# Kernel optimization log

Hardware: AMD Instinct MI355X
Metric: run time of the kernel (lower is better)

## Reference

```python
import jax, jax.numpy as jnp
import numpy as np

B, T, L, D = 4, 8, 512, 512
H, KD, VD = 8, 64, 64


def setup_inputs() -> dict:
    key = jax.random.key(0)
    ks = jax.random.split(key, 8)
    s = 0.05
    return {
        "queries": jax.random.normal(ks[0], (B, T, L, D), jnp.float32),
        "keys": jax.random.normal(ks[1], (B, T, L, D), jnp.float32),
        "values": jax.random.normal(ks[2], (B, T, L, D), jnp.float32),
        "attn_mask": jnp.ones((1, 1, 1, L, L), jnp.float32),
        "Wq": jax.random.normal(ks[3], (D, H, KD), jnp.float32) * s,
        "Wk": jax.random.normal(ks[4], (D, H, KD), jnp.float32) * s,
        "Wv": jax.random.normal(ks[5], (D, H, VD), jnp.float32) * s,
        "w_head": jax.random.normal(ks[6], (H,), jnp.float32),
        "tau": jnp.ones((1,), jnp.float32),
        "delta": jnp.zeros((1,), jnp.float32),
    }


def reference(queries, keys, values, attn_mask, Wq, Wk, Wv, w_head, tau, delta):
    # Projections: (b,t,l,d) x (d,h,e) -> (b,t,l,h,e)
    Q = jnp.einsum('btld,dhe->btlhe', queries, Wq)
    K = jnp.einsum('btld,dhe->btlhe', keys, Wk)
    V = jnp.einsum('btld,dhe->btlhe', values, Wv)
    scale = 1.0 / jnp.sqrt(jnp.asarray(KD, jnp.float32))
    # Full score tensor (b,t,h,l,s)
    scores = jnp.einsum('btlhe,btshe->bthls', Q, K)
    # de-stationary rescaling, then scale, then multiplicative mask
    scores = (scores * tau[0] + delta[0]) * scale
    scores = scores * attn_mask
    # Dropout(attn_dropout) before softmax is identity at inference
    p = jax.nn.softmax(scores, axis=-1)
    attn = jnp.einsum('bthls,btshe->bthle', p, V)
    # Per-head scalar weighted sum over heads: (b,t,h,l,e),(h)->(b,t,l,e)
    return jnp.einsum('bthle,h->btle', attn, w_head)
```

## Files before the change

kernel.cpp:

```cpp
#include <hip/hip_runtime.h>
#include <hip/hip_bf16.h>

typedef __bf16 bf16;
typedef __bf16 bf16x4 __attribute__((ext_vector_type(4)));
typedef __bf16 bf16x8 __attribute__((ext_vector_type(8)));
typedef float f32x4 __attribute__((ext_vector_type(4)));
typedef _Float16 half4 __attribute__((ext_vector_type(4)));


#if __has_builtin(__builtin_amdgcn_exp2f)
#define EXP2(x) __builtin_amdgcn_exp2f(x)
#else
#define EXP2(x) exp2f(x)
#endif

static __device__ __forceinline__ f32x4 mfma16(bf16x4 a, bf16x4 b, f32x4 c) {
#if __has_builtin(__builtin_amdgcn_mfma_f32_16x16x16bf16_1k)
    return __builtin_amdgcn_mfma_f32_16x16x16bf16_1k(a, b, c, 0, 0, 0);
#else
    asm("v_mfma_f32_16x16x16_bf16 %0, %1, %2, %0" : "+v"(c) : "v"(a), "v"(b));
    return c;
#endif
}

#if __has_builtin(__builtin_amdgcn_global_load_lds)
#define HAVE_GLL 1
#else
#define HAVE_GLL 0
#endif

static __device__ __forceinline__ void gll16(const void* gp, void* lbase, int lane) {
#if HAVE_GLL
    __builtin_amdgcn_global_load_lds(
        (const __attribute__((address_space(1))) void*)gp,
        (__attribute__((address_space(3))) void*)lbase, 16, 0, 0);
#else
    *(uint4*)((char*)lbase + lane * 16) = *(const uint4*)gp;
#endif
}

static __device__ __forceinline__ void prep_w_job(int job, const float* W0,
                                                  const float* W1, const float* W2,
                                                  bf16* Wt, char* sraw) {
    float(*t)[65] = (float(*)[65])sraw;
    const int z = job >> 6, sub = job & 63;
    const float* W = (z == 0) ? W0 : (z == 1) ? W1 : W2;
    bf16* O = Wt + (size_t)z * 512 * 512;
    const int d0 = (sub & 7) * 64, n0 = (sub >> 3) * 64;
    {
        int nl = threadIdx.x & 63, dg = threadIdx.x >> 6;
#pragma unroll
        for (int j = 0; j < 16; ++j) {
            int dl = dg + j * 4;
            t[nl][dl] = W[(size_t)(d0 + dl) * 512 + n0 + nl];
        }
    }
    __syncthreads();
    {
        int dl = threadIdx.x & 63, ng = threadIdx.x >> 6;
#pragma unroll
        for (int j = 0; j < 16; ++j) {
            int nl = ng + j * 4;
            O[(size_t)(n0 + nl) * 512 + d0 + dl] = (bf16)t[nl][dl];
        }
    }
}

static __device__ __forceinline__ void prep_mask_job(int bid, const float* maskf,
                                                     bf16* Mp) {
    const int t0 = bid * 256 + threadIdx.x;
    const float4* m4 = (const float4*)maskf;
#pragma unroll
    for (int j = 0; j < 4; ++j) {
        int idx = t0 + j * 16384;
        int q = idx >> 7;
        int sc = idx & 127;
        int cc = sc >> 4;
        int ns = (sc >> 2) & 3;
        int qd = sc & 3;
        float4 v = m4[idx];
        bf16x4 o;
        o[0] = (bf16)v.x; o[1] = (bf16)v.y; o[2] = (bf16)v.z; o[3] = (bf16)v.w;
        size_t off = ((((size_t)(q >> 4) * 8 + cc) * 4 + ns) * 4 + qd) * 64 +
                     (q & 15) * 4;
        *(bf16x4*)&Mp[off] = o;
    }
}

__global__ __launch_bounds__(256) void prep_kernel(const float* W0, const float* W1,
                                                   const float* W2, const float* maskf,
                                                   bf16* Wt, bf16* Mp) {
    __shared__ __align__(16) char sraw[16640];
    if (blockIdx.z == 3) {
        prep_mask_job(blockIdx.y * 8 + blockIdx.x, maskf, Mp);
        return;
    }
    prep_w_job(blockIdx.z * 64 + blockIdx.y * 8 + blockIdx.x, W0, W1, W2, Wt, sraw);
}

static __device__ __forceinline__ void proj_job(int j, const float* __restrict__ Xq,
                                                const float* __restrict__ Xk,
                                                const float* __restrict__ Xv,
                                                const bf16* __restrict__ Wt,
                                                bf16* __restrict__ Qw,
                                                bf16* __restrict__ Kw,
                                                bf16* __restrict__ Vt, char* sraw) {
    bf16* la = (bf16*)sraw;
    bf16* lb = (bf16*)sraw + 9216;

    const int z = j >> 9, bid = j & 511;
    const float* X = (z == 0) ? Xq : (z == 1) ? Xk : Xv;
    const bf16* W  = Wt + (size_t)z * 512 * 512;
    bf16* Out      = (z == 0) ? Qw : (z == 1) ? Kw : Vt;

    const int tid = threadIdx.x, wave = tid >> 6, lane = tid & 63;
    const int quad = lane >> 4, lc = lane & 15;
    const int wm = wave & 1, wn = wave >> 1;
    const int jj = bid >> 3;
    const int yy = jj & 3;
    const int xt = (bid & 7) * 16 + (jj >> 2);
    const int m0 = xt * 128, n0 = yy * 128;

    f32x4 acc[4][4];
#pragma unroll
    for (int ms = 0; ms < 4; ++ms)
#pragma unroll
        for (int ns = 0; ns < 4; ++ns) acc[ms][ns] = (f32x4){0.f, 0.f, 0.f, 0.f};

    const int ar = tid >> 4, ac = tid & 15;
    const int brl   = lane >> 3;
    const int bslot = lane & 7;
    const int bchunk = bslot ^ brl;

    float4 xr[8];
#pragma unroll
    for (int i = 0; i < 8; ++i)
        xr[i] = *(const float4*)&X[(size_t)(m0 + ar + i * 16) * 512 + ac * 4];

    for (int kb = 0; kb < 512; kb += 64) {
        __syncthreads();
#pragma unroll
        for (int i = 0; i < 4; ++i) {
            int rgrp = wave * 8 + i * 32;
            gll16(&W[(size_t)(n0 + rgrp + brl) * 512 + kb + bchunk * 8],
                  lb + (size_t)rgrp * 64, lane);
        }
#pragma unroll
        for (int i = 0; i < 8; ++i) {
            float4 x = xr[i];
            bf16x4 p;
            p[0] = (bf16)x.x; p[1] = (bf16)x.y; p[2] = (bf16)x.z; p[3] = (bf16)x.w;
            *(bf16x4*)&la[(ar + i * 16) * 72 + ac * 4] = p;
        }
#if HAVE_GLL
        asm volatile("s_waitcnt vmcnt(0)" ::: "memory");
#endif
        __syncthreads();
        if (kb < 448) {
            int kn = kb + 64;
#pragma unroll
            for (int i = 0; i < 8; ++i)
                xr[i] = *(const float4*)&X[(size_t)(m0 + ar + i * 16) * 512 + kn + ac * 4];
        }
#pragma unroll
        for (int kk = 0; kk < 2; ++kk) {
            bf16x8 af[4], bfr[4];
#pragma unroll
            for (int ms = 0; ms < 4; ++ms)
                af[ms] = *(bf16x8*)&la[(wm * 64 + ms * 16 + lc) * 72 + kk * 32 + quad * 8];
#pragma unroll
            for (int ns = 0; ns < 4; ++ns) {
                int row = wn * 64 + ns * 16 + lc;
                int slot = (kk * 4 + quad) ^ (lc & 7);
                bfr[ns] = *(bf16x8*)&lb[(size_t)row * 64 + slot * 8];
            }
#pragma unroll
            for (int ms = 0; ms < 4; ++ms)
#pragma unroll
                for (int ns = 0; ns < 4; ++ns)
                    acc[ms][ns] = __builtin_amdgcn_mfma_f32_16x16x32_bf16(
                        af[ms], bfr[ns], acc[ms][ns], 0, 0, 0);
        }
    }
    __syncthreads();
    bf16* lds_c = (bf16*)sraw;
    if (z != 2) {
#pragma unroll
        for (int ms = 0; ms < 4; ++ms)
#pragma unroll
            for (int ns = 0; ns < 4; ++ns)
#pragma unroll
                for (int r = 0; r < 4; ++r)
                    lds_c[(wm * 64 + ms * 16 + quad * 4 + r) * 136 +
                          wn * 64 + ns * 16 + lc] = (bf16)acc[ms][ns][r];
    } else {
#pragma unroll
        for (int ms = 0; ms < 4; ++ms)
#pragma unroll
            for (int ns = 0; ns < 4; ++ns)
#pragma unroll
                for (int r = 0; r < 4; ++r)
                    lds_c[(wn * 64 + ns * 16 + lc) * 136 +
                          wm * 64 + ms * 16 + quad * 4 + r] = (bf16)acc[ms][ns][r];
    }
    __syncthreads();
    const int bt = m0 >> 9, l0 = m0 & 511;
    if (z != 2) {
        const int ec = tid & 7, rg = tid >> 3;
#pragma unroll
        for (int hc = 0; hc < 2; ++hc) {
            int h = (n0 >> 6) + hc;
#pragma unroll
            for (int p = 0; p < 4; ++p) {
                int row = rg + p * 32;
                bf16x8 v = *(bf16x8*)&lds_c[row * 136 + hc * 64 + ec * 8];
                *(bf16x8*)&Out[(((size_t)bt * 8 + h) * 512 + l0 + row) * 64 + ec * 8] = v;
            }
        }
    } else {
        const int rowp = lane >> 2, cc = lane & 3;
#pragma unroll
        for (int pr = 0; pr < 2; ++pr) {
            int row = wave * 32 + pr * 16 + rowp;
            int h = (n0 >> 6) + (row >> 6);
            int e = row & 63;
            bf16* dst = Out + (((size_t)bt * 8 + h) * 64 + e) * 512 + l0;
#pragma unroll
            for (int pc = 0; pc < 4; ++pc) {
                int mc = cc + pc * 4;
                *(bf16x8*)&dst[mc * 8] = *(bf16x8*)&lds_c[row * 136 + mc * 8];
            }
        }
    }
}

__global__ __launch_bounds__(256) void proj_kernel(const float* Xq, const float* Xk,
                                                   const float* Xv, const bf16* Wt,
                                                   bf16* Qw, bf16* Kw, bf16* Vt) {
    __shared__ __align__(16) char sraw[34816];
    int j = blockIdx.z * 512 + blockIdx.y * 128 + blockIdx.x;
    proj_job(j, Xq, Xk, Xv, Wt, Qw, Kw, Vt, sraw);
}

__global__ __launch_bounds__(256, 4) void attn_kernel(
    const bf16* __restrict__ Qw, const bf16* __restrict__ Kw,
    const bf16* __restrict__ Vt, const bf16* __restrict__ Mp,
    const float* __restrict__ w_head, const float* __restrict__ tau,
    const float* __restrict__ delta, float* __restrict__ out,
    void* __restrict__ opart, int mode) {
    __shared__ __align__(16) bf16 lds_k[2][64 * 72];
    __shared__ __align__(16) bf16 lds_vt[2][64 * 72];

    const int tid  = threadIdx.x;
    const int wave = tid >> 6;
    const int lane = tid & 63;
    const int quad = lane >> 4;
    const int lc   = lane & 15;
    const int b    = blockIdx.x;
    const int bth  = b & 255;
    const int qquad = b >> 8;
    const int bt   = bth >> 3;
    const int h    = bth & 7;

    const bf16* Qh  = Qw + (size_t)bth * (512 * 64);
    const bf16* Kh  = Kw + (size_t)bth * (512 * 64);
    const bf16* VtH = Vt + (size_t)bth * (512 * 64);

    const float L2E = 1.4426950408889634f;
    const float ts = tau[0] * 0.125f * L2E;
    const float ds = delta[0] * 0.125f * L2E;
    const float wh = w_head[h];

    const int q0 = qquad * 128 + wave * 32;
    const size_t mbA = (size_t)(q0 >> 4) * 8192 + lane * 4;
    const size_t mbB = mbA + 8192;

    bf16x8 qfA[2], qfB[2];
#pragma unroll
    for (int kk = 0; kk < 2; ++kk) {
        qfA[kk] = *(const bf16x8*)&Qh[(size_t)(q0 + lc) * 64 + kk * 32 + quad * 8];
        qfB[kk] = *(const bf16x8*)&Qh[(size_t)(q0 + 16 + lc) * 64 + kk * 32 + quad * 8];
    }

    f32x4 oA[4], oB[4];
#pragma unroll
    for (int ns = 0; ns < 4; ++ns) {
        oA[ns] = (f32x4){0.f, 0.f, 0.f, 0.f};
        oB[ns] = (f32x4){0.f, 0.f, 0.f, 0.f};
    }
    float lA = 0.f, lB = 0.f;

    const int srow = tid >> 3, scc = tid & 7;
    bf16x8 kr[2], vr[2];
    kr[0] = *(const bf16x8*)&Kh[(size_t)srow * 64 + scc * 8];
    kr[1] = *(const bf16x8*)&Kh[(size_t)(srow + 32) * 64 + scc * 8];
    vr[0] = *(const bf16x8*)&VtH[(size_t)srow * 512 + scc * 8];
    vr[1] = *(const bf16x8*)&VtH[(size_t)(srow + 32) * 512 + scc * 8];
    *(bf16x8*)&lds_k[0][srow * 72 + scc * 8] = kr[0];
    *(bf16x8*)&lds_k[0][(srow + 32) * 72 + scc * 8] = kr[1];
    *(bf16x8*)&lds_vt[0][srow * 72 + scc * 8] = vr[0];
    *(bf16x8*)&lds_vt[0][(srow + 32) * 72 + scc * 8] = vr[1];
    kr[0] = *(const bf16x8*)&Kh[(size_t)(64 + srow) * 64 + scc * 8];
    kr[1] = *(const bf16x8*)&Kh[(size_t)(64 + srow + 32) * 64 + scc * 8];
    vr[0] = *(const bf16x8*)&VtH[(size_t)srow * 512 + 64 + scc * 8];
    vr[1] = *(const bf16x8*)&VtH[(size_t)(srow + 32) * 512 + 64 + scc * 8];

    for (int c = 0; c < 8; ++c) {
        const int buf = c & 1;
        __syncthreads();
        bf16x4 mA[4], mB[4];
        {
            const size_t mc = mbA + (size_t)c * 1024;
            const size_t md = mbB + (size_t)c * 1024;
#pragma unroll
            for (int ns = 0; ns < 4; ++ns) {
                mA[ns] = *(const bf16x4*)&Mp[mc + ns * 256];
                mB[ns] = *(const bf16x4*)&Mp[md + ns * 256];
            }
        }
        f32x4 stA[4], stB[4];
#pragma unroll
        for (int ns = 0; ns < 4; ++ns) {
            stA[ns] = (f32x4){0.f, 0.f, 0.f, 0.f};
            stB[ns] = (f32x4){0.f, 0.f, 0.f, 0.f};
        }
#pragma unroll
        for (int kk = 0; kk < 2; ++kk)
#pragma unroll
            for (int ns = 0; ns < 4; ++ns) {
                bf16x8 ka = *(bf16x8*)&lds_k[buf][(ns * 16 + lc) * 72 + kk * 32 + quad * 8];
                stA[ns] = __builtin_amdgcn_mfma_f32_16x16x32_bf16(ka, qfA[kk], stA[ns], 0, 0, 0);
                stB[ns] = __builtin_amdgcn_mfma_f32_16x16x32_bf16(ka, qfB[kk], stB[ns], 0, 0, 0);
            }
        if (c < 7) {
            const int nb = buf ^ 1;
            *(bf16x8*)&lds_k[nb][srow * 72 + scc * 8] = kr[0];
            *(bf16x8*)&lds_k[nb][(srow + 32) * 72 + scc * 8] = kr[1];
            *(bf16x8*)&lds_vt[nb][srow * 72 + scc * 8] = vr[0];
            *(bf16x8*)&lds_vt[nb][(srow + 32) * 72 + scc * 8] = vr[1];
            if (c < 6) {
                const int s0n = (c + 2) * 64;
                kr[0] = *(const bf16x8*)&Kh[(size_t)(s0n + srow) * 64 + scc * 8];
                kr[1] = *(const bf16x8*)&Kh[(size_t)(s0n + srow + 32) * 64 + scc * 8];
                vr[0] = *(const bf16x8*)&VtH[(size_t)srow * 512 + s0n + scc * 8];
                vr[1] = *(const bf16x8*)&VtH[(size_t)(srow + 32) * 512 + s0n + scc * 8];
            }
        }
        bf16x4 paA[4], paB[4];
#pragma unroll
        for (int ns = 0; ns < 4; ++ns) {
#pragma unroll
            for (int r = 0; r < 4; ++r) {
                float eA = (stA[ns][r] * ts + ds) * (float)mA[ns][r];
                float eB = (stB[ns][r] * ts + ds) * (float)mB[ns][r];
                float pA = EXP2(eA);
                float pB = EXP2(eB);
                lA += pA; lB += pB;
                paA[ns][r] = (bf16)pA;
                paB[ns][r] = (bf16)pB;
            }
        }
#pragma unroll
        for (int ks = 0; ks < 4; ++ks)
#pragma unroll
            for (int ns = 0; ns < 4; ++ns) {
                bf16x4 vv = *(bf16x4*)&lds_vt[buf][(ns * 16 + lc) * 72 + ks * 16 + quad * 4];
                oA[ns] = mfma16(paA[ks], vv, oA[ns]);
                oB[ns] = mfma16(paB[ks], vv, oB[ns]);
            }
    }
    lA += __shfl_xor(lA, 16, 64);
    lA += __shfl_xor(lA, 32, 64);
    lB += __shfl_xor(lB, 16, 64);
    lB += __shfl_xor(lB, 32, 64);
#pragma unroll
    for (int r = 0; r < 4; ++r) {
        float lrA = __shfl(lA, quad * 4 + r, 64);
        float lrB = __shfl(lB, quad * 4 + r, 64);
        float ivA = wh / lrA, ivB = wh / lrB;
        int qqA = q0 + quad * 4 + r;
        int qqB = q0 + 16 + quad * 4 + r;
        if (mode == 0) {
#pragma unroll
            for (int ns = 0; ns < 4; ++ns) {
                int e = ns * 16 + lc;
                atomicAdd(&out[((size_t)bt * 512 + qqA) * 64 + e], oA[ns][r] * ivA);
                atomicAdd(&out[((size_t)bt * 512 + qqB) * 64 + e], oB[ns][r] * ivB);
            }
        } else if (mode == 1) {
            float* op = (float*)opart;
#pragma unroll
            for (int ns = 0; ns < 4; ++ns) {
                int e = ns * 16 + lc;
                op[((size_t)bth * 512 + qqA) * 64 + e] = oA[ns][r] * ivA;
                op[((size_t)bth * 512 + qqB) * 64 + e] = oB[ns][r] * ivB;
            }
        } else {
            _Float16* op = (_Float16*)opart;
#pragma unroll
            for (int ns = 0; ns < 4; ++ns) {
                int e = ns * 16 + lc;
                op[((size_t)bth * 512 + qqA) * 64 + e] = (_Float16)(oA[ns][r] * ivA);
                op[((size_t)bth * 512 + qqB) * 64 + e] = (_Float16)(oB[ns][r] * ivB);
            }
        }
    }
}

__global__ __launch_bounds__(256) void reduce_kernel(const void* __restrict__ part,
                                                     float* __restrict__ out,
                                                     int mode) {
    const int idx = blockIdx.x * 256 + threadIdx.x;
    const int bt = idx >> 13;
    const int rf = idx & 8191;
    f32x4 s = (f32x4){0.f, 0.f, 0.f, 0.f};
    if (mode == 1) {
        const f32x4* p = (const f32x4*)part + (size_t)bt * 65536 + rf;
#pragma unroll
        for (int h = 0; h < 8; ++h) s += p[(size_t)h * 8192];
    } else {
        const half4* p = (const half4*)part + (size_t)bt * 65536 + rf;
#pragma unroll
        for (int h = 0; h < 8; ++h) {
            half4 v = p[(size_t)h * 8192];
            s[0] += (float)v[0]; s[1] += (float)v[1];
            s[2] += (float)v[2]; s[3] += (float)v[3];
        }
    }
    *(f32x4*)&out[(size_t)idx * 4] = s;
}

extern "C" void kernel_launch(void* const* d_in, const int* in_sizes, int n_in,
                              void* d_out, int out_size, void* d_ws, size_t ws_size,
                              hipStream_t stream) {
    const float* queries = (const float*)d_in[0];
    const float* keys    = (const float*)d_in[1];
    const float* values  = (const float*)d_in[2];
    const float* mask    = (const float*)d_in[3];
    const float* Wq      = (const float*)d_in[4];
    const float* Wk      = (const float*)d_in[5];
    const float* Wv      = (const float*)d_in[6];
    const float* w_head  = (const float*)d_in[7];
    const float* tau     = (const float*)d_in[8];
    const float* delta   = (const float*)d_in[9];

    char* ws = (char*)d_ws;
    bf16* Qw = (bf16*)(ws);
    bf16* Kw = (bf16*)(ws + 16777216ull);
    bf16* Vt = (bf16*)(ws + 33554432ull);
    bf16* Wt = (bf16*)(ws + 50331648ull);
    bf16* Mp = (bf16*)(ws + 51904512ull);
    char* Op = ws + 52428800ull;

    int mode = (ws_size >= 52428800ull + 33554432ull) ? 1
             : (ws_size >= 52428800ull + 16777216ull) ? 2 : 0;

    if (mode == 0)
        hipMemsetAsync(d_out, 0, (size_t)out_size * sizeof(float), stream);

    prep_kernel<<<dim3(8, 8, 4), 256, 0, stream>>>(Wq, Wk, Wv, mask, Wt, Mp);

    proj_kernel<<<dim3(128, 4, 3), 256, 0, stream>>>(queries, keys, values, Wt,
                                                     Qw, Kw, Vt);

    attn_kernel<<<1024, 256, 0, stream>>>(Qw, Kw, Vt, Mp, w_head, tau, delta,
                                          (float*)d_out, (void*)Op, mode);

    if (mode != 0)
        reduce_kernel<<<1024, 256, 0, stream>>>((const void*)Op, (float*)d_out,
                                                mode);
}
```

Before: 228.2 us.

## Fuse head reduction into attention kernel via last-block atomic counter

Removes the separate reduce kernel. Each attention block writes its fp32 per-head partial, then bumps an atomic counter per (bt, query-quarter). The last of the eight head blocks to arrive sums all heads and writes the output. The counter is zeroed in the prep kernel. This saves one kernel launch and lets the reduction overlap with attention tail work, at the cost of fences, atomics and a serial reduction done by the last block. The fp16 partial mode is dropped.

```diff
diff --git a/kernel.cpp b/kernel.cpp
--- a/kernel.cpp
+++ b/kernel.cpp
@@ -5,7 +5,6 @@
 typedef __bf16 bf16x4 __attribute__((ext_vector_type(4)));
 typedef __bf16 bf16x8 __attribute__((ext_vector_type(8)));
 typedef float f32x4 __attribute__((ext_vector_type(4)));
-typedef _Float16 half4 __attribute__((ext_vector_type(4)));
 
 
 #if __has_builtin(__builtin_amdgcn_exp2f)
@@ -89,8 +88,12 @@
 
 __global__ __launch_bounds__(256) void prep_kernel(const float* W0, const float* W1,
                                                    const float* W2, const float* maskf,
-                                                   bf16* Wt, bf16* Mp) {
+                                                   bf16* Wt, bf16* Mp,
+                                                   unsigned* cnt, int zero_cnt) {
     __shared__ __align__(16) char sraw[16640];
+    if (zero_cnt && blockIdx.z == 0 && blockIdx.y == 0 && blockIdx.x == 0 &&
+        threadIdx.x < 128)
+        cnt[threadIdx.x] = 0u;
     if (blockIdx.z == 3) {
         prep_mask_job(blockIdx.y * 8 + blockIdx.x, maskf, Mp);
         return;
@@ -247,9 +250,10 @@
     const bf16* __restrict__ Vt, const bf16* __restrict__ Mp,
     const float* __restrict__ w_head, const float* __restrict__ tau,
     const float* __restrict__ delta, float* __restrict__ out,
-    void* __restrict__ opart, int mode) {
+    float* __restrict__ opart, unsigned* __restrict__ cnt, int mode) {
     __shared__ __align__(16) bf16 lds_k[2][64 * 72];
     __shared__ __align__(16) bf16 lds_vt[2][64 * 72];
+    __shared__ int is_last;
 
     const int tid  = threadIdx.x;
     const int wave = tid >> 6;
@@ -387,47 +391,39 @@
                 atomicAdd(&out[((size_t)bt * 512 + qqA) * 64 + e], oA[ns][r] * ivA);
                 atomicAdd(&out[((size_t)bt * 512 + qqB) * 64 + e], oB[ns][r] * ivB);
             }
-        } else if (mode == 1) {
-            float* op = (float*)opart;
+        } else {
 #pragma unroll
             for (int ns = 0; ns < 4; ++ns) {
                 int e = ns * 16 + lc;
-                op[((size_t)bth * 512 + qqA) * 64 + e] = oA[ns][r] * ivA;
-                op[((size_t)bth * 512 + qqB) * 64 + e] = oB[ns][r] * ivB;
-            }
-        } else {
-            _Float16* op = (_Float16*)opart;
-#pragma unroll
-            for (int ns = 0; ns < 4; ++ns) {
-                int e = ns * 16 + lc;
-                op[((size_t)bth * 512 + qqA) * 64 + e] = (_Float16)(oA[ns][r] * ivA);
-                op[((size_t)bth * 512 + qqB) * 64 + e] = (_Float16)(oB[ns][r] * ivB);
-            }
-        }
-    }
-}
-
-__global__ __launch_bounds__(256) void reduce_kernel(const void* __restrict__ part,
-                                                     float* __restrict__ out,
-                                                     int mode) {
-    const int idx = blockIdx.x * 256 + threadIdx.x;
-    const int bt = idx >> 13;
-    const int rf = idx & 8191;
-    f32x4 s = (f32x4){0.f, 0.f, 0.f, 0.f};
-    if (mode == 1) {
-        const f32x4* p = (const f32x4*)part + (size_t)bt * 65536 + rf;
-#pragma unroll
-        for (int h = 0; h < 8; ++h) s += p[(size_t)h * 8192];
-    } else {
-        const half4* p = (const half4*)part + (size_t)bt * 65536 + rf;
-#pragma unroll
-        for (int h = 0; h < 8; ++h) {
-            half4 v = p[(size_t)h * 8192];
-            s[0] += (float)v[0]; s[1] += (float)v[1];
-            s[2] += (float)v[2]; s[3] += (float)v[3];
-        }
-    }
-    *(f32x4*)&out[(size_t)idx * 4] = s;
+                opart[((size_t)bth * 512 + qqA) * 64 + e] = oA[ns][r] * ivA;
+                opart[((size_t)bth * 512 + qqB) * 64 + e] = oB[ns][r] * ivB;
+            }
+        }
+    }
+    if (mode == 0) return;
+
+    __threadfence();
+    __syncthreads();
+    if (tid == 0) {
+        unsigned old = atomicAdd(&cnt[(bt << 2) | qquad], 1u);
+        is_last = (old == 7u) ? 1 : 0;
+    }
+    __syncthreads();
+    if (!is_last) return;
+    __threadfence();
+    const f32x4* p = (const f32x4*)opart;
+    const int qbase = qquad * 128;
+#pragma unroll
+    for (int k = 0; k < 8; ++k) {
+        int t = tid + k * 256;
+        int q = qbase + (t >> 4);
+        int e4 = t & 15;
+        f32x4 s = (f32x4){0.f, 0.f, 0.f, 0.f};
+#pragma unroll
+        for (int hh = 0; hh < 8; ++hh)
+            s += p[(size_t)(bt * 8 + hh) * 8192 + (size_t)q * 16 + e4];
+        *(f32x4*)&out[(((size_t)bt * 512 + q) * 64) + e4 * 4] = s;
+    }
 }
 
 extern "C" void kernel_launch(void* const* d_in, const int* in_sizes, int n_in,
@@ -450,23 +446,20 @@
     bf16* Vt = (bf16*)(ws + 33554432ull);
     bf16* Wt = (bf16*)(ws + 50331648ull);
     bf16* Mp = (bf16*)(ws + 51904512ull);
-    char* Op = ws + 52428800ull;
-
-    int mode = (ws_size >= 52428800ull + 33554432ull) ? 1
-             : (ws_size >= 52428800ull + 16777216ull) ? 2 : 0;
+    float* Op = (float*)(ws + 52428800ull);
+    unsigned* cnt = (unsigned*)(ws + 85983232ull);
+
+    int mode = (ws_size >= 85983232ull + 512ull) ? 1 : 0;
 
     if (mode == 0)
         hipMemsetAsync(d_out, 0, (size_t)out_size * sizeof(float), stream);
 
-    prep_kernel<<<dim3(8, 8, 4), 256, 0, stream>>>(Wq, Wk, Wv, mask, Wt, Mp);
+    prep_kernel<<<dim3(8, 8, 4), 256, 0, stream>>>(Wq, Wk, Wv, mask, Wt, Mp,
+                                                   cnt, mode);
 
     proj_kernel<<<dim3(128, 4, 3), 256, 0, stream>>>(queries, keys, values, Wt,
                                                      Qw, Kw, Vt);
 
     attn_kernel<<<1024, 256, 0, stream>>>(Qw, Kw, Vt, Mp, w_head, tau, delta,
-                                          (float*)d_out, (void*)Op, mode);
-
-    if (mode != 0)
-        reduce_kernel<<<1024, 256, 0, stream>>>((const void*)Op, (float*)d_out,
-                                                mode);
-}
+                                          (float*)d_out, Op, cnt, mode);
+}
```

Measured after the change: 402.4 us. +76.3%, slower.
